# Kernel optimization log

Hardware: AMD Instinct MI355X
Metric: run time of the kernel (lower is better)

The kernel has to match this reference:

```python
import jax, jax.numpy as jnp
import numpy as np

NUM_CLASSES = 80
IMG_DIM = 2048
WORD_DIM = 300
INTER = 1024


def _branch(fmap, word, W1, W2, W3, b3, Wa, ba):
    # fmap: [B, C, H, W] -> [B, H, W, C]  (matches torch transpose(1,2),(2,3))
    x = jnp.transpose(fmap, (0, 2, 3, 1))
    fw = jnp.einsum('bhwc,dc->bhwd', x, W1)          # [B,H,W,d]
    fd = jnp.einsum('kw,dw->kd', word, W2)            # [K,d]
    # broadcast instead of repeat: tanh-gated bilinear feature [B,H,W,K,d]
    t = jnp.tanh(fw[:, :, :, None, :] * fd[None, None, None, :, :])
    lb = jnp.einsum('bhwkd,ed->bhwke', t, W3) + b3    # [B,H,W,K,d]
    score = jnp.einsum('bhwkd,od->bhwko', lb, Wa)[..., 0] + ba[0]  # [B,H,W,K]
    B, H, W, K = score.shape
    coeff = jax.nn.softmax(score.reshape(B, H * W, K), axis=1).reshape(B, H, W, K)
    # weighted spatial sum pooling per class -> [B, K, C]
    return jnp.einsum('bhwk,bhwc->bkc', coeff, x)


def setup_inputs() -> dict:
    key = jax.random.key(0)
    ks = jax.random.split(key, 12)
    d2 = INTER // 2
    s = 0.02
    return {
        'batch_size': 4,
        'stage_3_img_feature_map': jax.random.normal(ks[0], (4, IMG_DIM // 2, 28, 28), jnp.float32),
        'stage_4_img_feature_map': jax.random.normal(ks[1], (4, IMG_DIM, 14, 14), jnp.float32),
        'word_features': jax.random.normal(ks[2], (NUM_CLASSES, WORD_DIM), jnp.float32),
        # stage-3 branch params (torch Linear weight layout [out, in])
        'W1_s3': jax.random.normal(ks[3], (d2, IMG_DIM // 2), jnp.float32) * s,
        'W2_s3': jax.random.normal(ks[4], (d2, WORD_DIM), jnp.float32) * s,
        'W3_s3': jax.random.normal(ks[5], (d2, d2), jnp.float32) * s,
        'b3_s3': jnp.zeros((d2,), jnp.float32),
        'Wa_s3': jax.random.normal(ks[6], (1, d2), jnp.float32) * s,
        'ba_s3': jnp.zeros((1,), jnp.float32),
        # stage-4 branch params
        'W1_s4': jax.random.normal(ks[7], (INTER, IMG_DIM), jnp.float32) * s,
        'W2_s4': jax.random.normal(ks[8], (INTER, WORD_DIM), jnp.float32) * s,
        'W3_s4': jax.random.normal(ks[9], (INTER, INTER), jnp.float32) * s,
        'b3_s4': jnp.zeros((INTER,), jnp.float32),
        'Wa_s4': jax.random.normal(ks[10], (1, INTER), jnp.float32) * s,
        'ba_s4': jnp.zeros((1,), jnp.float32),
    }


def reference(batch_size, stage_3_img_feature_map, stage_4_img_feature_map, word_features,
              W1_s3, W2_s3, W3_s3, b3_s3, Wa_s3, ba_s3,
              W1_s4, W2_s4, W3_s4, b3_s4, Wa_s4, ba_s4):
    out3 = _branch(stage_3_img_feature_map, word_features, W1_s3, W2_s3, W3_s3, b3_s3, Wa_s3, ba_s3)
    out4 = _branch(stage_4_img_feature_map, word_features, W1_s4, W2_s4, W3_s4, b3_s4, Wa_s4, ba_s4)
    return (out3, out4)
```

## Files before the change

### kernel.cpp

```cpp
#include <hip/hip_runtime.h>

#define K_CLS 80
#define WDIM  300

typedef __attribute__((ext_vector_type(8))) short s16x8;
typedef __attribute__((ext_vector_type(4))) float f32x4;

__device__ inline unsigned short f2bf(float x) {
    unsigned int u = __builtin_bit_cast(unsigned int, x);
    unsigned int r = (u + 0x7fffu + ((u >> 16) & 1u)) >> 16;
    return (unsigned short)r;
}

__global__ __launch_bounds__(256) void k_small(
    const float* __restrict__ word,
    const float* __restrict__ W23, float* __restrict__ fd3,
    const float* __restrict__ W24, float* __restrict__ fd4,
    const float* __restrict__ Wa3, const float* __restrict__ W33, float* __restrict__ v3,
    const float* __restrict__ Wa4, const float* __restrict__ W34, float* __restrict__ v4) {
    __shared__ float red[4][64];
    int bid = blockIdx.x;
    int t = threadIdx.x;
    if (bid < 480) {
        const float* W2; float* fd; int D, base;
        if (bid < 160) { W2 = W23; fd = fd3; D = 512; base = bid; }
        else           { W2 = W24; fd = fd4; D = 1024; base = bid - 160; }
        int idx = base * 256 + t;
        int k = idx / D;
        int d = idx - k * D;
        const float4* wr = (const float4*)(word + (size_t)k * WDIM);
        const float4* w2 = (const float4*)(W2 + (size_t)d * WDIM);
        float acc = 0.f;
#pragma unroll 5
        for (int j = 0; j < WDIM / 4; ++j) {
            float4 a = wr[j], b = w2[j];
            acc += a.x * b.x + a.y * b.y + a.z * b.z + a.w * b.w;
        }
        fd[idx] = acc * 2.885390081777927f;
    } else {
        const float* Wa; const float* W3; float* v; int D, vblk;
        if (bid < 488) { Wa = Wa3; W3 = W33; v = v3; D = 512; vblk = bid - 480; }
        else           { Wa = Wa4; W3 = W34; v = v4; D = 1024; vblk = bid - 488; }
        int d0 = vblk * 64;
        int dl = t & 63, eg = t >> 6;
        float a[8] = {};
        int nIt = D >> 5;
        for (int i = 0; i < nIt; ++i) {
            int e0 = eg + 32 * i;
#pragma unroll
            for (int j = 0; j < 8; ++j)
                a[j] = fmaf(Wa[e0 + 4 * j], W3[(size_t)(e0 + 4 * j) * D + d0 + dl], a[j]);
        }
        float s = ((a[0] + a[1]) + (a[2] + a[3])) + ((a[4] + a[5]) + (a[6] + a[7]));
        red[eg][dl] = s;
        __syncthreads();
        if (t < 64) v[d0 + t] = red[0][t] + red[1][t] + red[2][t] + red[3][t];
    }
}

__global__ __launch_bounds__(256) void k_fw(
    const float* __restrict__ fmap3, const float* __restrict__ W13, float* __restrict__ fw3,
    const float* __restrict__ fmap4, const float* __restrict__ W14, float* __restrict__ fw4) {
    __shared__ short Al[2][64 * 40];
    __shared__ short Bl[2][64 * 40];
    int gid = blockIdx.x;
    const float *fmap, *W1; float* fw; int C, HW, D, dnb, hwnb;
    if (gid < 416) { fmap = fmap3; W1 = W13; fw = fw3; C = 1024; HW = 784; D = 512;  dnb = 8;  hwnb = 13; }
    else { gid -= 416; fmap = fmap4; W1 = W14; fw = fw4; C = 2048; HW = 196; D = 1024; dnb = 16; hwnb = 4; }
    int dblk = gid % dnb; gid /= dnb;
    int hwblk = gid % hwnb;
    int b = gid / hwnb;
    int m0 = hwblk * 64, d0 = dblk * 64;
    int tid = threadIdx.x, wave = tid >> 6, lane = tid & 63;
    const float* fb = fmap + (size_t)b * C * HW;

    int am = tid & 63, ac0 = (tid >> 6) * 8;
    int bd = tid >> 2, bc0 = (tid & 3) * 8;
    int hwA = m0 + am;
    bool okA = hwA < HW;
    const float* aptr = fb + (size_t)ac0 * HW + (okA ? hwA : 0);
    const float* bptr = W1 + (size_t)(d0 + bd) * C + bc0;

    float ar[8];
    float4 br0, br1;
#pragma unroll
    for (int i = 0; i < 8; ++i) ar[i] = okA ? aptr[(size_t)i * HW] : 0.f;
    br0 = *(const float4*)(bptr);
    br1 = *(const float4*)(bptr + 4);

    f32x4 acc[4];
#pragma unroll
    for (int nr = 0; nr < 4; ++nr) acc[nr] = (f32x4){0.f, 0.f, 0.f, 0.f};

#define CW(bufi)                                                       \
    {                                                                  \
        s16x8 ap;                                                      \
        _Pragma("unroll") for (int i = 0; i < 8; ++i) ap[i] = (short)f2bf(ar[i]); \
        *(s16x8*)&Al[bufi][am * 40 + ac0] = ap;                        \
        s16x8 bp;                                                      \
        bp[0] = (short)f2bf(br0.x); bp[1] = (short)f2bf(br0.y);        \
        bp[2] = (short)f2bf(br0.z); bp[3] = (short)f2bf(br0.w);        \
        bp[4] = (short)f2bf(br1.x); bp[5] = (short)f2bf(br1.y);        \
        bp[6] = (short)f2bf(br1.z); bp[7] = (short)f2bf(br1.w);        \
        *(s16x8*)&Bl[bufi][bd * 40 + bc0] = bp;                        \
    }

    CW(0);
    __syncthreads();

    int NS = C >> 5;
    int ko = (lane >> 4) * 8, rr = lane & 15;
    for (int s = 0; s < NS; ++s) {
        if (s + 1 < NS) {
            int nk = (s + 1) * 32;
            const float* ap2 = aptr + (size_t)nk * HW;
#pragma unroll
            for (int i = 0; i < 8; ++i) ar[i] = okA ? ap2[(size_t)i * HW] : 0.f;
            br0 = *(const float4*)(bptr + nk);
            br1 = *(const float4*)(bptr + nk + 4);
        }
        int buf = s & 1;
        s16x8 afr = *(s16x8*)&Al[buf][(wave * 16 + rr) * 40 + ko];
        s16x8 bfr[4];
#pragma unroll
        for (int nr = 0; nr < 4; ++nr)
            bfr[nr] = *(s16x8*)&Bl[buf][(nr * 16 + rr) * 40 + ko];
#pragma unroll
        for (int nr = 0; nr < 4; ++nr)
            acc[nr] = __builtin_amdgcn_mfma_f32_16x16x32_bf16(afr, bfr[nr], acc[nr], 0, 0, 0);
        if (s + 1 < NS) CW(buf ^ 1);
        __syncthreads();
    }

    int row4 = (lane >> 4) * 4, col = lane & 15;
#pragma unroll
    for (int j = 0; j < 4; ++j) {
        int mm = m0 + wave * 16 + row4 + j;
        if (mm < HW) {
#pragma unroll
            for (int nr = 0; nr < 4; ++nr)
                fw[((size_t)b * HW + mm) * D + d0 + nr * 16 + col] = acc[nr][j];
        }
    }
#undef CW
}

__global__ __launch_bounds__(320) void k_score(
    const float* __restrict__ fw3, const float* __restrict__ fd3,
    const float* __restrict__ v3, float* __restrict__ p3,
    const float* __restrict__ fw4, const float* __restrict__ fd4,
    const float* __restrict__ v4, float* __restrict__ p4) {
    __shared__ float fwl[4][1024];
    __shared__ float vl[1024];
    int bid = blockIdx.x;
    const float *fw, *fd, *v; float* p; int D, HW;
    if (bid < 784) { fw = fw3; fd = fd3; v = v3; p = p3; D = 512; HW = 784; }
    else { bid -= 784; fw = fw4; fd = fd4; v = v4; p = p4; D = 1024; HW = 196; }
    int nt = HW >> 2;
    int b = bid / nt, m0 = (bid - b * nt) * 4;
    int tid = threadIdx.x;
    const float* fwg = fw + ((size_t)b * HW + m0) * D;
    for (int i = tid; i < D; i += 320) {
        vl[i] = v[i];
#pragma unroll
        for (int t2 = 0; t2 < 4; ++t2) fwl[t2][i] = fwg[(size_t)t2 * D + i];
    }
    __syncthreads();
    int wave = tid >> 6, lane = tid & 63;
    int kk = lane >> 2, ds = lane & 3;
    int k = wave * 16 + kk;
    int DS = D >> 2;
    const float4* fdp = (const float4*)(fd + (size_t)k * D + ds * DS);
    const float4* vp  = (const float4*)(vl + ds * DS);
    int n4 = DS >> 2;
    for (int t = 0; t < 4; ++t) {
        const float4* fwp = (const float4*)(&fwl[t][ds * DS]);
        float a0 = 0.f, a1 = 0.f, a2 = 0.f, a3 = 0.f;
        for (int j = 0; j < n4; j += 4) {
            float4 f0 = fdp[j], f1 = fdp[j + 1], f2 = fdp[j + 2], f3 = fdp[j + 3];
            float4 w0 = fwp[j], w1 = fwp[j + 1], w2 = fwp[j + 2], w3 = fwp[j + 3];
            float4 v0 = vp[j], v1 = vp[j + 1], v2 = vp[j + 2], v3_ = vp[j + 3];
            a0 += v0.x * __builtin_amdgcn_rcpf(__builtin_amdgcn_exp2f(w0.x * f0.x) + 1.f)
                + v0.y * __builtin_amdgcn_rcpf(__builtin_amdgcn_exp2f(w0.y * f0.y) + 1.f)
                + v0.z * __builtin_amdgcn_rcpf(__builtin_amdgcn_exp2f(w0.z * f0.z) + 1.f)
                + v0.w * __builtin_amdgcn_rcpf(__builtin_amdgcn_exp2f(w0.w * f0.w) + 1.f);
            a1 += v1.x * __builtin_amdgcn_rcpf(__builtin_amdgcn_exp2f(w1.x * f1.x) + 1.f)
                + v1.y * __builtin_amdgcn_rcpf(__builtin_amdgcn_exp2f(w1.y * f1.y) + 1.f)
                + v1.z * __builtin_amdgcn_rcpf(__builtin_amdgcn_exp2f(w1.z * f1.z) + 1.f)
                + v1.w * __builtin_amdgcn_rcpf(__builtin_amdgcn_exp2f(w1.w * f1.w) + 1.f);
            a2 += v2.x * __builtin_amdgcn_rcpf(__builtin_amdgcn_exp2f(w2.x * f2.x) + 1.f)
                + v2.y * __builtin_amdgcn_rcpf(__builtin_amdgcn_exp2f(w2.y * f2.y) + 1.f)
                + v2.z * __builtin_amdgcn_rcpf(__builtin_amdgcn_exp2f(w2.z * f2.z) + 1.f)
                + v2.w * __builtin_amdgcn_rcpf(__builtin_amdgcn_exp2f(w2.w * f2.w) + 1.f);
            a3 += v3_.x * __builtin_amdgcn_rcpf(__builtin_amdgcn_exp2f(w3.x * f3.x) + 1.f)
                + v3_.y * __builtin_amdgcn_rcpf(__builtin_amdgcn_exp2f(w3.y * f3.y) + 1.f)
                + v3_.z * __builtin_amdgcn_rcpf(__builtin_amdgcn_exp2f(w3.z * f3.z) + 1.f)
                + v3_.w * __builtin_amdgcn_rcpf(__builtin_amdgcn_exp2f(w3.w * f3.w) + 1.f);
        }
        float acc = (a0 + a1) + (a2 + a3);
        acc += __shfl_xor(acc, 1);
        acc += __shfl_xor(acc, 2);
        if (ds == 0)
            p[((size_t)b * K_CLS + k) * HW + m0 + t] =
                __builtin_amdgcn_exp2f(acc * -2.885390081777927f);
    }
}

#define CHUNK 128
__global__ __launch_bounds__(256) void k_pool(
    const float* __restrict__ p3, const float* __restrict__ fmap3,
    const float* __restrict__ p4, const float* __restrict__ fmap4,
    float* __restrict__ out) {
    __shared__ float pl[40][CHUNK];
    __shared__ float fl[32][CHUNK + 1];
    int bid = blockIdx.x;
    const float *p, *fmap; float* o; int C, HW;
    if (bid < 256) { p = p3; fmap = fmap3; o = out; C = 1024; HW = 784; }
    else { bid -= 256; p = p4; fmap = fmap4; o = out + (size_t)4 * K_CLS * 1024; C = 2048; HW = 196; }
    int cnb = C >> 5;
    int c0 = (bid % cnb) * 32; bid /= cnb;
    int kb = (bid & 1) * 40;
    int b = bid >> 1;
    int tid = threadIdx.x;
    int c_l = tid & 31;
    int k_l = (tid >> 5) * 5;
    const float* fb = fmap + (size_t)b * C * HW;
    float acc[5] = {}, ps[5] = {};
    for (int hw0 = 0; hw0 < HW; hw0 += CHUNK) {
        for (int idx = tid; idx < 40 * CHUNK; idx += 256) {
            int r = idx >> 7, cc = idx & (CHUNK - 1);
            int hw = hw0 + cc;
            pl[r][cc] = (hw < HW) ? p[((size_t)b * K_CLS + kb + r) * HW + hw] : 0.f;
        }
        for (int idx = tid; idx < 32 * CHUNK; idx += 256) {
            int r = idx >> 7, cc = idx & (CHUNK - 1);
            int hw = hw0 + cc;
            fl[r][cc] = (hw < HW) ? fb[(size_t)(c0 + r) * HW + hw] : 0.f;
        }
        __syncthreads();
#pragma unroll 4
        for (int j = 0; j < CHUNK; ++j) {
            float fv = fl[c_l][j];
#pragma unroll
            for (int t = 0; t < 5; ++t) {
                float pv = pl[k_l + t][j];
                acc[t] += pv * fv;
                ps[t] += pv;
            }
        }
        __syncthreads();
    }
#pragma unroll
    for (int t = 0; t < 5; ++t) {
        int k = kb + k_l + t;
        o[((size_t)b * K_CLS + k) * C + c0 + c_l] = acc[t] / ps[t];
    }
}

extern "C" void kernel_launch(void* const* d_in, const int* in_sizes, int n_in,
                              void* d_out, int out_size, void* d_ws, size_t ws_size,
                              hipStream_t stream) {
    const float* fmap3 = (const float*)d_in[1];
    const float* fmap4 = (const float*)d_in[2];
    const float* word  = (const float*)d_in[3];
    const float* W1_3  = (const float*)d_in[4];
    const float* W2_3  = (const float*)d_in[5];
    const float* W3_3  = (const float*)d_in[6];
    const float* Wa_3  = (const float*)d_in[8];
    const float* W1_4  = (const float*)d_in[10];
    const float* W2_4  = (const float*)d_in[11];
    const float* W3_4  = (const float*)d_in[12];
    const float* Wa_4  = (const float*)d_in[14];
    float* out = (float*)d_out;

    float* ws = (float*)d_ws;
    size_t off = 0;
    float* fw3 = ws + off; off += (size_t)3136 * 512;
    float* fd3 = ws + off; off += (size_t)80 * 512;
    float* v3  = ws + off; off += 512;
    float* sc3 = ws + off; off += (size_t)4 * 80 * 784;
    float* fw4 = ws + off; off += (size_t)784 * 1024;
    float* fd4 = ws + off; off += (size_t)80 * 1024;
    float* v4  = ws + off; off += 1024;
    float* sc4 = ws + off; off += (size_t)4 * 80 * 196;

    k_small<<<504, 256, 0, stream>>>(word, W2_3, fd3, W2_4, fd4,
                                     Wa_3, W3_3, v3, Wa_4, W3_4, v4);
    k_fw<<<672, 256, 0, stream>>>(fmap3, W1_3, fw3, fmap4, W1_4, fw4);
    k_score<<<980, 320, 0, stream>>>(fw3, fd3, v3, sc3, fw4, fd4, v4, sc4);
    k_pool<<<768, 256, 0, stream>>>(sc3, fmap3, sc4, fmap4, out);
}
```

Before: 354.4 us.

## Retile fd, fw GEMM and score kernels for more per-thread reuse

k_small now has each thread compute four class rows of fd, so every W2 row load is reused across four word vectors. k_fw moves to 512-thread blocks with a 128-row HW tile, which halves the grid and shares each W1 tile across more rows. k_score drops the split-D loop over four positions and instead accumulates all four spatial positions together, reusing each fd/v load four times and loading the shared tiles with float4. The cost is fewer blocks and therefore less parallelism, plus extra padded rows in the larger fw tile for HW=196.

```diff
diff --git a/kernel.cpp b/kernel.cpp
--- a/kernel.cpp
+++ b/kernel.cpp
@@ -4,12 +4,24 @@
 #define WDIM  300
 
 typedef __attribute__((ext_vector_type(8))) short s16x8;
+typedef __attribute__((ext_vector_type(4))) short s16x4;
 typedef __attribute__((ext_vector_type(4))) float f32x4;
 
 __device__ inline unsigned short f2bf(float x) {
     unsigned int u = __builtin_bit_cast(unsigned int, x);
     unsigned int r = (u + 0x7fffu + ((u >> 16) & 1u)) >> 16;
     return (unsigned short)r;
+}
+
+__device__ inline float dot4(float4 a, float4 b) {
+    return a.x * b.x + a.y * b.y + a.z * b.z + a.w * b.w;
+}
+
+__device__ inline float t4(float4 wv, float4 fv, float4 vv) {
+    return vv.x * __builtin_amdgcn_rcpf(__builtin_amdgcn_exp2f(wv.x * fv.x) + 1.f)
+         + vv.y * __builtin_amdgcn_rcpf(__builtin_amdgcn_exp2f(wv.y * fv.y) + 1.f)
+         + vv.z * __builtin_amdgcn_rcpf(__builtin_amdgcn_exp2f(wv.z * fv.z) + 1.f)
+         + vv.w * __builtin_amdgcn_rcpf(__builtin_amdgcn_exp2f(wv.w * fv.w) + 1.f);
 }
 
 __global__ __launch_bounds__(256) void k_small(
@@ -21,26 +33,35 @@
     __shared__ float red[4][64];
     int bid = blockIdx.x;
     int t = threadIdx.x;
-    if (bid < 480) {
-        const float* W2; float* fd; int D, base;
-        if (bid < 160) { W2 = W23; fd = fd3; D = 512; base = bid; }
-        else           { W2 = W24; fd = fd4; D = 1024; base = bid - 160; }
-        int idx = base * 256 + t;
-        int k = idx / D;
-        int d = idx - k * D;
-        const float4* wr = (const float4*)(word + (size_t)k * WDIM);
-        const float4* w2 = (const float4*)(W2 + (size_t)d * WDIM);
-        float acc = 0.f;
+    if (bid < 120) {
+        const float* W2; float* fd; int D, kt, dblk;
+        if (bid < 40) { W2 = W23; fd = fd3; D = 512; kt = bid >> 1; dblk = bid & 1; }
+        else { int i2 = bid - 40; W2 = W24; fd = fd4; D = 1024; kt = i2 >> 2; dblk = i2 & 3; }
+        int d = dblk * 256 + t;
+        int k0 = kt * 4;
+        const float4* w2p = (const float4*)(W2 + (size_t)d * WDIM);
+        const float4* wr0 = (const float4*)(word + (size_t)(k0 + 0) * WDIM);
+        const float4* wr1 = (const float4*)(word + (size_t)(k0 + 1) * WDIM);
+        const float4* wr2 = (const float4*)(word + (size_t)(k0 + 2) * WDIM);
+        const float4* wr3 = (const float4*)(word + (size_t)(k0 + 3) * WDIM);
+        float a0 = 0.f, a1 = 0.f, a2 = 0.f, a3 = 0.f;
 #pragma unroll 5
         for (int j = 0; j < WDIM / 4; ++j) {
-            float4 a = wr[j], b = w2[j];
-            acc += a.x * b.x + a.y * b.y + a.z * b.z + a.w * b.w;
-        }
-        fd[idx] = acc * 2.885390081777927f;
+            float4 w = w2p[j];
+            a0 += dot4(wr0[j], w);
+            a1 += dot4(wr1[j], w);
+            a2 += dot4(wr2[j], w);
+            a3 += dot4(wr3[j], w);
+        }
+        const float S = 2.885390081777927f;
+        fd[(size_t)(k0 + 0) * D + d] = a0 * S;
+        fd[(size_t)(k0 + 1) * D + d] = a1 * S;
+        fd[(size_t)(k0 + 2) * D + d] = a2 * S;
+        fd[(size_t)(k0 + 3) * D + d] = a3 * S;
     } else {
         const float* Wa; const float* W3; float* v; int D, vblk;
-        if (bid < 488) { Wa = Wa3; W3 = W33; v = v3; D = 512; vblk = bid - 480; }
-        else           { Wa = Wa4; W3 = W34; v = v4; D = 1024; vblk = bid - 488; }
+        if (bid < 128) { Wa = Wa3; W3 = W33; v = v3; D = 512; vblk = bid - 120; }
+        else           { Wa = Wa4; W3 = W34; v = v4; D = 1024; vblk = bid - 128; }
         int d0 = vblk * 64;
         int dl = t & 63, eg = t >> 6;
         float a[8] = {};
@@ -58,51 +79,48 @@
     }
 }
 
-__global__ __launch_bounds__(256) void k_fw(
+__global__ __launch_bounds__(512) void k_fw(
     const float* __restrict__ fmap3, const float* __restrict__ W13, float* __restrict__ fw3,
     const float* __restrict__ fmap4, const float* __restrict__ W14, float* __restrict__ fw4) {
-    __shared__ short Al[2][64 * 40];
+    __shared__ short Al[2][128 * 40];
     __shared__ short Bl[2][64 * 40];
     int gid = blockIdx.x;
     const float *fmap, *W1; float* fw; int C, HW, D, dnb, hwnb;
-    if (gid < 416) { fmap = fmap3; W1 = W13; fw = fw3; C = 1024; HW = 784; D = 512;  dnb = 8;  hwnb = 13; }
-    else { gid -= 416; fmap = fmap4; W1 = W14; fw = fw4; C = 2048; HW = 196; D = 1024; dnb = 16; hwnb = 4; }
+    if (gid < 224) { fmap = fmap3; W1 = W13; fw = fw3; C = 1024; HW = 784; D = 512;  dnb = 8;  hwnb = 7; }
+    else { gid -= 224; fmap = fmap4; W1 = W14; fw = fw4; C = 2048; HW = 196; D = 1024; dnb = 16; hwnb = 2; }
     int dblk = gid % dnb; gid /= dnb;
     int hwblk = gid % hwnb;
     int b = gid / hwnb;
-    int m0 = hwblk * 64, d0 = dblk * 64;
+    int m0 = hwblk * 128, d0 = dblk * 64;
     int tid = threadIdx.x, wave = tid >> 6, lane = tid & 63;
     const float* fb = fmap + (size_t)b * C * HW;
 
-    int am = tid & 63, ac0 = (tid >> 6) * 8;
-    int bd = tid >> 2, bc0 = (tid & 3) * 8;
+    int am = tid & 127, ac0 = (tid >> 7) * 8;
+    int bd = tid >> 3, bc0 = (tid & 7) * 4;
     int hwA = m0 + am;
     bool okA = hwA < HW;
     const float* aptr = fb + (size_t)ac0 * HW + (okA ? hwA : 0);
     const float* bptr = W1 + (size_t)(d0 + bd) * C + bc0;
 
     float ar[8];
-    float4 br0, br1;
+    float4 br;
 #pragma unroll
     for (int i = 0; i < 8; ++i) ar[i] = okA ? aptr[(size_t)i * HW] : 0.f;
-    br0 = *(const float4*)(bptr);
-    br1 = *(const float4*)(bptr + 4);
+    br = *(const float4*)bptr;
 
     f32x4 acc[4];
 #pragma unroll
     for (int nr = 0; nr < 4; ++nr) acc[nr] = (f32x4){0.f, 0.f, 0.f, 0.f};
 
-#define CW(bufi)                                                       \
-    {                                                                  \
-        s16x8 ap;                                                      \
+#define CW(bufi)                                                              \
+    {                                                                         \
+        s16x8 ap;                                                             \
         _Pragma("unroll") for (int i = 0; i < 8; ++i) ap[i] = (short)f2bf(ar[i]); \
-        *(s16x8*)&Al[bufi][am * 40 + ac0] = ap;                        \
-        s16x8 bp;                                                      \
-        bp[0] = (short)f2bf(br0.x); bp[1] = (short)f2bf(br0.y);        \
-        bp[2] = (short)f2bf(br0.z); bp[3] = (short)f2bf(br0.w);        \
-        bp[4] = (short)f2bf(br1.x); bp[5] = (short)f2bf(br1.y);        \
-        bp[6] = (short)f2bf(br1.z); bp[7] = (short)f2bf(br1.w);        \
-        *(s16x8*)&Bl[bufi][bd * 40 + bc0] = bp;                        \
+        *(s16x8*)&Al[bufi][am * 40 + ac0] = ap;                               \
+        s16x4 bp;                                                             \
+        bp[0] = (short)f2bf(br.x); bp[1] = (short)f2bf(br.y);                 \
+        bp[2] = (short)f2bf(br.z); bp[3] = (short)f2bf(br.w);                 \
+        *(s16x4*)&Bl[bufi][bd * 40 + bc0] = bp;                               \
     }
 
     CW(0);
@@ -112,12 +130,10 @@
     int ko = (lane >> 4) * 8, rr = lane & 15;
     for (int s = 0; s < NS; ++s) {
         if (s + 1 < NS) {
-            int nk = (s + 1) * 32;
-            const float* ap2 = aptr + (size_t)nk * HW;
+            const float* ap2 = aptr + (size_t)(s + 1) * 32 * HW;
 #pragma unroll
             for (int i = 0; i < 8; ++i) ar[i] = okA ? ap2[(size_t)i * HW] : 0.f;
-            br0 = *(const float4*)(bptr + nk);
-            br1 = *(const float4*)(bptr + nk + 4);
+            br = *(const float4*)(bptr + (s + 1) * 32);
         }
         int buf = s & 1;
         s16x8 afr = *(s16x8*)&Al[buf][(wave * 16 + rr) * 40 + ko];
@@ -131,6 +147,7 @@
         if (s + 1 < NS) CW(buf ^ 1);
         __syncthreads();
     }
+#undef CW
 
     int row4 = (lane >> 4) * 4, col = lane & 15;
 #pragma unroll
@@ -142,7 +159,6 @@
                 fw[((size_t)b * HW + mm) * D + d0 + nr * 16 + col] = acc[nr][j];
         }
     }
-#undef CW
 }
 
 __global__ __launch_bounds__(320) void k_score(
@@ -160,49 +176,45 @@
     int b = bid / nt, m0 = (bid - b * nt) * 4;
     int tid = threadIdx.x;
     const float* fwg = fw + ((size_t)b * HW + m0) * D;
-    for (int i = tid; i < D; i += 320) {
-        vl[i] = v[i];
-#pragma unroll
-        for (int t2 = 0; t2 < 4; ++t2) fwl[t2][i] = fwg[(size_t)t2 * D + i];
+    int D4 = D >> 2;
+    if (tid < D4) {
+        ((float4*)vl)[tid] = ((const float4*)v)[tid];
+#pragma unroll
+        for (int t = 0; t < 4; ++t)
+            ((float4*)fwl[t])[tid] = ((const float4*)(fwg + (size_t)t * D))[tid];
     }
     __syncthreads();
     int wave = tid >> 6, lane = tid & 63;
     int kk = lane >> 2, ds = lane & 3;
     int k = wave * 16 + kk;
-    int DS = D >> 2;
-    const float4* fdp = (const float4*)(fd + (size_t)k * D + ds * DS);
-    const float4* vp  = (const float4*)(vl + ds * DS);
-    int n4 = DS >> 2;
-    for (int t = 0; t < 4; ++t) {
-        const float4* fwp = (const float4*)(&fwl[t][ds * DS]);
-        float a0 = 0.f, a1 = 0.f, a2 = 0.f, a3 = 0.f;
-        for (int j = 0; j < n4; j += 4) {
-            float4 f0 = fdp[j], f1 = fdp[j + 1], f2 = fdp[j + 2], f3 = fdp[j + 3];
-            float4 w0 = fwp[j], w1 = fwp[j + 1], w2 = fwp[j + 2], w3 = fwp[j + 3];
-            float4 v0 = vp[j], v1 = vp[j + 1], v2 = vp[j + 2], v3_ = vp[j + 3];
-            a0 += v0.x * __builtin_amdgcn_rcpf(__builtin_amdgcn_exp2f(w0.x * f0.x) + 1.f)
-                + v0.y * __builtin_amdgcn_rcpf(__builtin_amdgcn_exp2f(w0.y * f0.y) + 1.f)
-                + v0.z * __builtin_amdgcn_rcpf(__builtin_amdgcn_exp2f(w0.z * f0.z) + 1.f)
-                + v0.w * __builtin_amdgcn_rcpf(__builtin_amdgcn_exp2f(w0.w * f0.w) + 1.f);
-            a1 += v1.x * __builtin_amdgcn_rcpf(__builtin_amdgcn_exp2f(w1.x * f1.x) + 1.f)
-                + v1.y * __builtin_amdgcn_rcpf(__builtin_amdgcn_exp2f(w1.y * f1.y) + 1.f)
-                + v1.z * __builtin_amdgcn_rcpf(__builtin_amdgcn_exp2f(w1.z * f1.z) + 1.f)
-                + v1.w * __builtin_amdgcn_rcpf(__builtin_amdgcn_exp2f(w1.w * f1.w) + 1.f);
-            a2 += v2.x * __builtin_amdgcn_rcpf(__builtin_amdgcn_exp2f(w2.x * f2.x) + 1.f)
-                + v2.y * __builtin_amdgcn_rcpf(__builtin_amdgcn_exp2f(w2.y * f2.y) + 1.f)
-                + v2.z * __builtin_amdgcn_rcpf(__builtin_amdgcn_exp2f(w2.z * f2.z) + 1.f)
-                + v2.w * __builtin_amdgcn_rcpf(__builtin_amdgcn_exp2f(w2.w * f2.w) + 1.f);
-            a3 += v3_.x * __builtin_amdgcn_rcpf(__builtin_amdgcn_exp2f(w3.x * f3.x) + 1.f)
-                + v3_.y * __builtin_amdgcn_rcpf(__builtin_amdgcn_exp2f(w3.y * f3.y) + 1.f)
-                + v3_.z * __builtin_amdgcn_rcpf(__builtin_amdgcn_exp2f(w3.z * f3.z) + 1.f)
-                + v3_.w * __builtin_amdgcn_rcpf(__builtin_amdgcn_exp2f(w3.w * f3.w) + 1.f);
-        }
-        float acc = (a0 + a1) + (a2 + a3);
-        acc += __shfl_xor(acc, 1);
-        acc += __shfl_xor(acc, 2);
-        if (ds == 0)
-            p[((size_t)b * K_CLS + k) * HW + m0 + t] =
-                __builtin_amdgcn_exp2f(acc * -2.885390081777927f);
+    const float4* fdp = (const float4*)(fd + (size_t)k * D);
+    const float4* vp  = (const float4*)vl;
+    const float4* w0p = (const float4*)fwl[0];
+    const float4* w1p = (const float4*)fwl[1];
+    const float4* w2p = (const float4*)fwl[2];
+    const float4* w3p = (const float4*)fwl[3];
+    float acc0 = 0.f, acc1 = 0.f, acc2 = 0.f, acc3 = 0.f;
+    int NJ = D >> 4;
+    for (int jj = 0; jj < NJ; jj += 2) {
+        int c0 = jj * 4 + ds, c1 = c0 + 4;
+        float4 f0 = fdp[c0], f1 = fdp[c1];
+        float4 va = vp[c0], vb = vp[c1];
+        acc0 += t4(w0p[c0], f0, va) + t4(w0p[c1], f1, vb);
+        acc1 += t4(w1p[c0], f0, va) + t4(w1p[c1], f1, vb);
+        acc2 += t4(w2p[c0], f0, va) + t4(w2p[c1], f1, vb);
+        acc3 += t4(w3p[c0], f0, va) + t4(w3p[c1], f1, vb);
+    }
+    acc0 += __shfl_xor(acc0, 1); acc0 += __shfl_xor(acc0, 2);
+    acc1 += __shfl_xor(acc1, 1); acc1 += __shfl_xor(acc1, 2);
+    acc2 += __shfl_xor(acc2, 1); acc2 += __shfl_xor(acc2, 2);
+    acc3 += __shfl_xor(acc3, 1); acc3 += __shfl_xor(acc3, 2);
+    if (ds == 0) {
+        const float S = -2.885390081777927f;
+        float* pr = p + ((size_t)b * K_CLS + k) * HW + m0;
+        pr[0] = __builtin_amdgcn_exp2f(acc0 * S);
+        pr[1] = __builtin_amdgcn_exp2f(acc1 * S);
+        pr[2] = __builtin_amdgcn_exp2f(acc2 * S);
+        pr[3] = __builtin_amdgcn_exp2f(acc3 * S);
     }
 }
 
@@ -284,9 +296,9 @@
     float* v4  = ws + off; off += 1024;
     float* sc4 = ws + off; off += (size_t)4 * 80 * 196;
 
-    k_small<<<504, 256, 0, stream>>>(word, W2_3, fd3, W2_4, fd4,
+    k_small<<<144, 256, 0, stream>>>(word, W2_3, fd3, W2_4, fd4,
                                      Wa_3, W3_3, v3, Wa_4, W3_4, v4);
-    k_fw<<<672, 256, 0, stream>>>(fmap3, W1_3, fw3, fmap4, W1_4, fw4);
+    k_fw<<<352, 512, 0, stream>>>(fmap3, W1_3, fw3, fmap4, W1_4, fw4);
     k_score<<<980, 320, 0, stream>>>(fw3, fd3, v3, sc3, fw4, fd4, v4, sc4);
     k_pool<<<768, 256, 0, stream>>>(sc3, fmap3, sc4, fmap4, out);
 }
```

New measurement: 315.6 us. -10.9%, faster.
